# Kernel tuning notes

Hardware: AMD Instinct MI355X
Metric: run time of the kernel (lower is better)

Reference implementation:

```python
import jax, jax.numpy as jnp
import numpy as np

D_MODEL = 1024
N_HEADS = 16
D_K = D_MODEL // N_HEADS


def setup_inputs() -> dict:
    key = jax.random.key(0)
    ks = jax.random.split(key, 7)
    B, T = 4, 2048
    scale = 1.0 / np.sqrt(D_MODEL)
    x = jax.random.normal(ks[0], (B, T, D_MODEL), dtype=jnp.float32)
    Wq = jax.random.uniform(ks[1], (D_MODEL, D_MODEL), jnp.float32, -scale, scale)
    Wk = jax.random.uniform(ks[2], (D_MODEL, D_MODEL), jnp.float32, -scale, scale)
    Wv = jax.random.uniform(ks[3], (D_MODEL, D_MODEL), jnp.float32, -scale, scale)
    bq = jax.random.uniform(ks[4], (D_MODEL,), jnp.float32, -scale, scale)
    bk = jax.random.uniform(ks[5], (D_MODEL,), jnp.float32, -scale, scale)
    bv = jax.random.uniform(ks[6], (D_MODEL,), jnp.float32, -scale, scale)
    return {"x": x, "Wq": Wq, "bq": bq, "Wk": Wk, "bk": bk, "Wv": Wv, "bv": bv}


def reference(x, Wq, bq, Wk, bk, Wv, bv):
    B, T, _ = x.shape
    # QKV projections -> (B, H, T, d_k)
    def split_heads(y):
        return y.reshape(B, T, N_HEADS, D_K).transpose(0, 2, 1, 3)
    Q = split_heads(x @ Wq + bq)
    K = split_heads(x @ Wk + bk)
    V = split_heads(x @ Wv + bv)
    scores = jnp.einsum('bhqd,bhkd->bhqk', Q, K) / jnp.sqrt(jnp.float32(D_K))
    # additive causal mask: -inf above the diagonal
    causal = jnp.tril(jnp.ones((T, T), dtype=bool))
    scores = jnp.where(causal, scores, -jnp.inf)
    attn = jax.nn.softmax(scores, axis=-1)
    out = jnp.einsum('bhqk,bhkd->bhqd', attn, V)
    return out.transpose(0, 2, 1, 3).reshape(B, T, D_MODEL)
```

## Files before the change

kernel.cpp:

```cpp
#include <hip/hip_runtime.h>
#include <hip/hip_bf16.h>

#define DM 1024
#define NH 16
#define DK 64
#define TT 2048
#define NBATCH 4
#define BT 8192

typedef __attribute__((ext_vector_type(8))) short short8;
typedef __attribute__((ext_vector_type(4))) float f32x4;
typedef unsigned short u16;

#define MFMA(a,b,c) __builtin_amdgcn_mfma_f32_16x16x32_bf16((a),(b),(c),0,0,0)

#define QSCALE 0.18033688011112684f

#define EXP2(x) __builtin_amdgcn_exp2f(x)

__device__ __forceinline__ u16 f2bf(float f){
  union { float f; unsigned u; } v; v.f = f;
  return (u16)((v.u + 0x7fffu + ((v.u >> 16) & 1u)) >> 16);
}

__device__ __forceinline__ unsigned cvtpk(float lo, float hi){
  unsigned r;
  asm("v_cvt_pk_bf16_f32 %0, %1, %2" : "=v"(r) : "v"(lo), "v"(hi));
  return r;
}

__device__ __forceinline__ void gload16(const void* g, void* l){
  __builtin_amdgcn_global_load_lds((__attribute__((address_space(1))) void*)(g),
                                   (__attribute__((address_space(3))) void*)(l), 16, 0, 0);
}

__device__ __forceinline__ float plmax(float x){
#if __has_builtin(__builtin_amdgcn_permlane16_swap) && __has_builtin(__builtin_amdgcn_permlane32_swap)
  auto r = __builtin_amdgcn_permlane16_swap(__float_as_uint(x), __float_as_uint(x), false, false);
  x = fmaxf(__uint_as_float(r[0]), __uint_as_float(r[1]));
  auto r2 = __builtin_amdgcn_permlane32_swap(__float_as_uint(x), __float_as_uint(x), false, false);
  x = fmaxf(__uint_as_float(r2[0]), __uint_as_float(r2[1]));
#else
  x = fmaxf(x, __shfl_xor(x, 16, 64));
  x = fmaxf(x, __shfl_xor(x, 32, 64));
#endif
  return x;
}

__device__ __forceinline__ float plsum(float x){
#if __has_builtin(__builtin_amdgcn_permlane16_swap) && __has_builtin(__builtin_amdgcn_permlane32_swap)
  auto r = __builtin_amdgcn_permlane16_swap(__float_as_uint(x), __float_as_uint(x), false, false);
  x = __uint_as_float(r[0]) + __uint_as_float(r[1]);
  auto r2 = __builtin_amdgcn_permlane32_swap(__float_as_uint(x), __float_as_uint(x), false, false);
  x = __uint_as_float(r2[0]) + __uint_as_float(r2[1]);
#else
  x = x + __shfl_xor(x, 16, 64);
  x = x + __shfl_xor(x, 32, 64);
#endif
  return x;
}

__global__ __launch_bounds__(256) void cvt_x(const float* __restrict__ x, u16* __restrict__ xb){
  int i = (blockIdx.x * 256 + threadIdx.x) * 4;
  float4 v = *(const float4*)(x + i);
  u16 o0 = f2bf(v.x), o1 = f2bf(v.y), o2 = f2bf(v.z), o3 = f2bf(v.w);
  ushort4 o; o.x=o0; o.y=o1; o.z=o2; o.w=o3;
  *(ushort4*)(xb + i) = o;
}

__global__ __launch_bounds__(256) void twp(
    const float* __restrict__ Wq, const float* __restrict__ Wk, const float* __restrict__ Wv,
    u16* __restrict__ wtq, u16* __restrict__ wtk, u16* __restrict__ wtv){
  const float* W = (blockIdx.z == 0) ? Wq : (blockIdx.z == 1) ? Wk : Wv;
  u16* wt = (blockIdx.z == 0) ? wtq : (blockIdx.z == 1) ? wtk : wtv;
  __shared__ float tile[32][33];
  int k0 = blockIdx.x * 32, n0 = blockIdx.y * 32;
  int tx = threadIdx.x & 31, ty = threadIdx.x >> 5;
  #pragma unroll
  for(int r = ty; r < 32; r += 8)
    tile[r][tx] = W[(size_t)(k0 + r) * DM + n0 + tx];
  __syncthreads();
  #pragma unroll
  for(int r = ty; r < 32; r += 8)
    wt[(size_t)(n0 + r) * DM + k0 + tx] = f2bf(tile[tx][r]);
}

__global__ __launch_bounds__(256) void qkv_gemm(
    const u16* __restrict__ xb,
    const u16* __restrict__ wtq, const u16* __restrict__ wtk, const u16* __restrict__ wtv,
    const float* __restrict__ bq, const float* __restrict__ bk, const float* __restrict__ bv,
    u16* __restrict__ qws, u16* __restrict__ kws, u16* __restrict__ vtws){
  __shared__ u16 sa[128 * 64];
  __shared__ u16 sb[128 * 64];
  const int m0 = blockIdx.x * 128;
  const int ng = blockIdx.y * 128;
  const int mat = ng >> 10;
  const int n0 = ng & 1023;
  const u16* wt = (mat == 0) ? wtq : (mat == 1) ? wtk : wtv;
  const float* bias = (mat == 0) ? bq : (mat == 1) ? bk : bv;
  const int tid = threadIdx.x;
  const int lane = tid & 63, w = tid >> 6;
  const int wm = (w >> 1) * 64, wn = (w & 1) * 64;
  const int wbase0 = tid & 192;

  f32x4 acc[4][4] = {};

  for(int k0 = 0; k0 < 1024; k0 += 64){
    #pragma unroll
    for(int p = 0; p < 4; p++){
      int base = p * 256 + wbase0;
      int idx = base + lane;
      int row = idx >> 3;
      int chs = (idx & 7) ^ (row & 7);
      gload16(xb + (size_t)(m0 + row) * 1024 + k0 + chs * 8, (char*)sa + base * 16);
      gload16(wt + (size_t)(n0 + row) * 1024 + k0 + chs * 8, (char*)sb + base * 16);
    }
    __syncthreads();
    #pragma unroll
    for(int ks = 0; ks < 2; ks++){
      short8 af[4], bfr[4];
      #pragma unroll
      for(int i = 0; i < 4; i++){
        int ra = wm + i * 16 + (lane & 15);
        int ca = ks * 64 + (lane >> 4) * 16;
        af[i] = *(const short8*)((const char*)sa + ra * 128 + (ca ^ ((ra & 7) << 4)));
        int rb = wn + i * 16 + (lane & 15);
        bfr[i] = *(const short8*)((const char*)sb + rb * 128 + (ca ^ ((rb & 7) << 4)));
      }
      __builtin_amdgcn_s_setprio(1);
      #pragma unroll
      for(int i = 0; i < 4; i++)
        #pragma unroll
        for(int j = 0; j < 4; j++)
          acc[i][j] = MFMA(af[i], bfr[j], acc[i][j]);
      __builtin_amdgcn_s_setprio(0);
    }
    __syncthreads();
  }

  const float scl = (mat == 0) ? QSCALE : 1.0f;
  #pragma unroll
  for(int j = 0; j < 4; j++){
    int n = n0 + wn + j * 16 + (lane & 15);
    float bv_ = bias[n];
    int h = n >> 6, d = n & 63;
    #pragma unroll
    for(int i = 0; i < 4; i++){
      int mb = m0 + wm + i * 16 + (lane >> 4) * 4;
      int b = mb >> 11, t = mb & 2047;
      int bh = b * NH + h;
      if(mat == 2){
        ushort4 o4;
        o4.x = f2bf(acc[i][j][0] + bv_);
        o4.y = f2bf(acc[i][j][1] + bv_);
        o4.z = f2bf(acc[i][j][2] + bv_);
        o4.w = f2bf(acc[i][j][3] + bv_);
        int tp = (t & ~31) | (((t >> 2) & 3) << 3) | (((t >> 4) & 1) << 2);
        *(ushort4*)(vtws + ((size_t)bh * DK + d) * TT + tp) = o4;
      } else {
        u16* dst = (mat == 0) ? qws : kws;
        #pragma unroll
        for(int r = 0; r < 4; r++){
          u16 o = f2bf((acc[i][j][r] + bv_) * scl);
          dst[((size_t)bh * TT + t + r) * DK + d] = o;
        }
      }
    }
  }
}

__global__ __launch_bounds__(256) void attn(
    const u16* __restrict__ qws, const u16* __restrict__ kws, const u16* __restrict__ vtws,
    float* __restrict__ out){
  __shared__ u16 kt[2][64 * 64];
  __shared__ u16 vt[2][64 * 64];

  const int id = blockIdx.x;
  const int swz = (id & 7) * 128 + (id >> 3);
  const int qx = swz & 15;
  const int bh = swz >> 4;

  const int tid = threadIdx.x, lane = tid & 63, w = tid >> 6;
  const int g = lane >> 4, ln = lane & 15;
  const int b = bh >> 4, h = bh & 15;
  const u16* kbase = kws + (size_t)bh * TT * DK;
  const u16* vbase = vtws + (size_t)bh * DK * TT;
  const int wbase0 = tid & 192;

  #pragma unroll 1
  for(int qi = 0; qi < 2; qi++){
    const int qt = qi ? (31 - qx) : qx;
    const int q = qt * 64 + w * 16 + ln;

    short8 qf[2];
    {
      const u16* gq = qws + ((size_t)bh * TT + q) * DK + g * 8;
      qf[0] = *(const short8*)gq;
      qf[1] = *(const short8*)(gq + 32);
    }

    f32x4 o[4] = {};
    float m = -INFINITY, l = 0.f;

    const int nkt = qt + 1;

    __syncthreads();
    #pragma unroll
    for(int p = 0; p < 2; p++){
      int base = p * 256 + wbase0;
      int idx = base + lane, row = idx >> 3, chs = (idx & 7) ^ (row & 7);
      gload16(kbase + (size_t)row * DK + chs * 8, (char*)kt[0] + base * 16);
      gload16(vbase + (size_t)row * TT + chs * 8, (char*)vt[0] + base * 16);
    }

    #pragma unroll 1
    for(int kti = 0; kti < nkt; kti++){
      const int cur = kti & 1;
      __syncthreads();

      if(kti + 1 < nkt){
        const int k0n = (kti + 1) * 64;
        #pragma unroll
        for(int p = 0; p < 2; p++){
          int base = p * 256 + wbase0;
          int idx = base + lane, row = idx >> 3, chs = (idx & 7) ^ (row & 7);
          gload16(kbase + (size_t)(k0n + row) * DK + chs * 8, (char*)kt[cur ^ 1] + base * 16);
          gload16(vbase + (size_t)row * TT + k0n + chs * 8, (char*)vt[cur ^ 1] + base * 16);
        }
      }

      f32x4 s[4];
      __builtin_amdgcn_s_setprio(1);
      #pragma unroll
      for(int i = 0; i < 4; i++){
        f32x4 c = {};
        #pragma unroll
        for(int ks = 0; ks < 2; ks++){
          int rb = i * 16 + ln;
          int cb = ks * 64 + g * 16;
          short8 kfr = *(const short8*)((const char*)kt[cur] + rb * 128 + (cb ^ ((rb & 7) << 4)));
          c = MFMA(kfr, qf[ks], c);
        }
        s[i] = c;
      }
      __builtin_amdgcn_s_setprio(0);

      if(kti == nkt - 1){
        const int k0 = kti * 64;
        #pragma unroll
        for(int i = 0; i < 4; i++)
          #pragma unroll
          for(int r = 0; r < 4; r++)
            if(k0 + i * 16 + g * 4 + r > q) s[i][r] = -INFINITY;
      }

      float mx0 = fmaxf(fmaxf(s[0][0], s[0][1]), fmaxf(s[0][2], s[0][3]));
      float mx1 = fmaxf(fmaxf(s[1][0], s[1][1]), fmaxf(s[1][2], s[1][3]));
      float mx2 = fmaxf(fmaxf(s[2][0], s[2][1]), fmaxf(s[2][2], s[2][3]));
      float mx3 = fmaxf(fmaxf(s[3][0], s[3][1]), fmaxf(s[3][2], s[3][3]));
      float pmax = fmaxf(fmaxf(mx0, mx1), fmaxf(mx2, mx3));
      pmax = plmax(pmax);

      if(!__all(pmax <= m + 8.f)){
        float mnew = fmaxf(m, pmax);
        float alpha = EXP2(m - mnew);
        l *= alpha;
        #pragma unroll
        for(int i = 0; i < 4; i++)
          #pragma unroll
          for(int r = 0; r < 4; r++) o[i][r] *= alpha;
        m = mnew;
      }

      #pragma unroll
      for(int i = 0; i < 4; i++)
        #pragma unroll
        for(int r = 0; r < 4; r++){
          float p = EXP2(s[i][r] - m);
          s[i][r] = p; l += p;
        }

      union PU { short8 s8; unsigned w[4]; };
      PU pb[2];
      #pragma unroll
      for(int ks = 0; ks < 2; ks++){
        pb[ks].w[0] = cvtpk(s[2*ks][0],   s[2*ks][1]);
        pb[ks].w[1] = cvtpk(s[2*ks][2],   s[2*ks][3]);
        pb[ks].w[2] = cvtpk(s[2*ks+1][0], s[2*ks+1][1]);
        pb[ks].w[3] = cvtpk(s[2*ks+1][2], s[2*ks+1][3]);
      }

      __builtin_amdgcn_s_setprio(1);
      #pragma unroll
      for(int i = 0; i < 4; i++){
        int dr = i * 16 + ln;
        const char* vrow = (const char*)vt[cur] + dr * 128;
        int sw = (dr & 7) << 4;
        #pragma unroll
        for(int ks = 0; ks < 2; ks++){
          short8 av = *(const short8*)(vrow + ((64 * ks + g * 16) ^ sw));
          o[i] = MFMA(av, pb[ks].s8, o[i]);
        }
      }
      __builtin_amdgcn_s_setprio(0);
    }

    l = plsum(l);
    float inv = 1.0f / l;
    float* orow = out + ((size_t)(b * TT + q)) * DM + h * 64 + g * 4;
    #pragma unroll
    for(int i = 0; i < 4; i++){
      float4 v4;
      v4.x = o[i][0] * inv; v4.y = o[i][1] * inv;
      v4.z = o[i][2] * inv; v4.w = o[i][3] * inv;
      *(float4*)(orow + i * 16) = v4;
    }
  }
}

extern "C" void kernel_launch(void* const* d_in, const int* in_sizes, int n_in,
                              void* d_out, int out_size, void* d_ws, size_t ws_size,
                              hipStream_t stream){
  const float* x  = (const float*)d_in[0];
  const float* Wq = (const float*)d_in[1];
  const float* bq = (const float*)d_in[2];
  const float* Wk = (const float*)d_in[3];
  const float* bk = (const float*)d_in[4];
  const float* Wv = (const float*)d_in[5];
  const float* bv = (const float*)d_in[6];
  float* out = (float*)d_out;

  char* ws = (char*)d_ws;
  u16* xb   = (u16*)(ws);
  u16* wtq  = (u16*)(ws + (16u << 20));
  u16* wtk  = (u16*)(ws + (18u << 20));
  u16* wtv  = (u16*)(ws + (20u << 20));
  u16* qws  = (u16*)(ws + (22u << 20));
  u16* kws  = (u16*)(ws + (38u << 20));
  u16* vtws = (u16*)(ws + (54u << 20));

  cvt_x<<<dim3(BT * DM / 1024), dim3(256), 0, stream>>>(x, xb);
  twp<<<dim3(32, 32, 3), dim3(256), 0, stream>>>(Wq, Wk, Wv, wtq, wtk, wtv);
  qkv_gemm<<<dim3(64, 24), dim3(256), 0, stream>>>(xb, wtq, wtk, wtv, bq, bk, bv, qws, kws, vtws);
  attn<<<dim3(1024), dim3(256), 0, stream>>>(qws, kws, vtws, out);
}
```

Before: 156.4 us.

## Use 128-query attention tiles with 8 waves and swizzle GEMM block order

The attention kernel now runs 512 threads per block and covers 128 queries, so each K/V tile loaded into shared memory serves eight waves instead of four. This halves K/V global traffic per query and gives each thread a single 16-byte load per tile. The first four waves skip the final diagonal tile, which they do not need under the causal mask. The QKV GEMM launch is flattened to 1D with an XCD-aware swizzle of tile order, aimed at better L2 reuse. In exchange the grid is half as large and the last key tile leaves half the waves idle.

```diff
diff --git a/kernel.cpp b/kernel.cpp
--- a/kernel.cpp
+++ b/kernel.cpp
@@ -92,8 +92,12 @@
     u16* __restrict__ qws, u16* __restrict__ kws, u16* __restrict__ vtws){
   __shared__ u16 sa[128 * 64];
   __shared__ u16 sb[128 * 64];
-  const int m0 = blockIdx.x * 128;
-  const int ng = blockIdx.y * 128;
+  const int id = blockIdx.x;
+  const int idx = id >> 3;
+  const int mt = (id & 7) * 8 + (idx & 7);
+  const int y  = idx >> 3;
+  const int m0 = mt * 128;
+  const int ng = y * 128;
   const int mat = ng >> 10;
   const int n0 = ng & 1023;
   const u16* wt = (mat == 0) ? wtq : (mat == 1) ? wtk : wtv;
@@ -109,9 +113,9 @@
     #pragma unroll
     for(int p = 0; p < 4; p++){
       int base = p * 256 + wbase0;
-      int idx = base + lane;
-      int row = idx >> 3;
-      int chs = (idx & 7) ^ (row & 7);
+      int idx2 = base + lane;
+      int row = idx2 >> 3;
+      int chs = (idx2 & 7) ^ (row & 7);
       gload16(xb + (size_t)(m0 + row) * 1024 + k0 + chs * 8, (char*)sa + base * 16);
       gload16(wt + (size_t)(n0 + row) * 1024 + k0 + chs * 8, (char*)sb + base * 16);
     }
@@ -169,28 +173,30 @@
   }
 }
 
-__global__ __launch_bounds__(256) void attn(
+__global__ __launch_bounds__(512) void attn(
     const u16* __restrict__ qws, const u16* __restrict__ kws, const u16* __restrict__ vtws,
     float* __restrict__ out){
   __shared__ u16 kt[2][64 * 64];
   __shared__ u16 vt[2][64 * 64];
 
   const int id = blockIdx.x;
-  const int swz = (id & 7) * 128 + (id >> 3);
-  const int qx = swz & 15;
-  const int bh = swz >> 4;
+  const int swz = (id & 7) * 64 + (id >> 3);
+  const int qx = swz & 7;
+  const int bh = swz >> 3;
 
   const int tid = threadIdx.x, lane = tid & 63, w = tid >> 6;
   const int g = lane >> 4, ln = lane & 15;
   const int b = bh >> 4, h = bh & 15;
   const u16* kbase = kws + (size_t)bh * TT * DK;
   const u16* vbase = vtws + (size_t)bh * DK * TT;
-  const int wbase0 = tid & 192;
+  const int sbase = tid & 448;
+  const int srow = tid >> 3;
+  const int schs = (tid & 7) ^ (srow & 7);
 
   #pragma unroll 1
   for(int qi = 0; qi < 2; qi++){
-    const int qt = qi ? (31 - qx) : qx;
-    const int q = qt * 64 + w * 16 + ln;
+    const int qt = qi ? (15 - qx) : qx;
+    const int q = qt * 128 + w * 16 + ln;
 
     short8 qf[2];
     {
@@ -202,16 +208,12 @@
     f32x4 o[4] = {};
     float m = -INFINITY, l = 0.f;
 
-    const int nkt = qt + 1;
+    const int nkt = 2 * qt + 2;
+    const int myNkt = nkt - (w < 4 ? 1 : 0);
 
     __syncthreads();
-    #pragma unroll
-    for(int p = 0; p < 2; p++){
-      int base = p * 256 + wbase0;
-      int idx = base + lane, row = idx >> 3, chs = (idx & 7) ^ (row & 7);
-      gload16(kbase + (size_t)row * DK + chs * 8, (char*)kt[0] + base * 16);
-      gload16(vbase + (size_t)row * TT + chs * 8, (char*)vt[0] + base * 16);
-    }
+    gload16(kbase + (size_t)srow * DK + schs * 8, (char*)kt[0] + sbase * 16);
+    gload16(vbase + (size_t)srow * TT + schs * 8, (char*)vt[0] + sbase * 16);
 
     #pragma unroll 1
     for(int kti = 0; kti < nkt; kti++){
@@ -220,89 +222,86 @@
 
       if(kti + 1 < nkt){
         const int k0n = (kti + 1) * 64;
-        #pragma unroll
-        for(int p = 0; p < 2; p++){
-          int base = p * 256 + wbase0;
-          int idx = base + lane, row = idx >> 3, chs = (idx & 7) ^ (row & 7);
-          gload16(kbase + (size_t)(k0n + row) * DK + chs * 8, (char*)kt[cur ^ 1] + base * 16);
-          gload16(vbase + (size_t)row * TT + k0n + chs * 8, (char*)vt[cur ^ 1] + base * 16);
-        }
+        gload16(kbase + (size_t)(k0n + srow) * DK + schs * 8, (char*)kt[cur ^ 1] + sbase * 16);
+        gload16(vbase + (size_t)srow * TT + k0n + schs * 8, (char*)vt[cur ^ 1] + sbase * 16);
       }
 
-      f32x4 s[4];
-      __builtin_amdgcn_s_setprio(1);
-      #pragma unroll
-      for(int i = 0; i < 4; i++){
-        f32x4 c = {};
+      if(kti < myNkt){
+        f32x4 s[4];
+        __builtin_amdgcn_s_setprio(1);
+        #pragma unroll
+        for(int i = 0; i < 4; i++){
+          f32x4 c = {};
+          #pragma unroll
+          for(int ks = 0; ks < 2; ks++){
+            int rb = i * 16 + ln;
+            int cb = ks * 64 + g * 16;
+            short8 kfr = *(const short8*)((const char*)kt[cur] + rb * 128 + (cb ^ ((rb & 7) << 4)));
+            c = MFMA(kfr, qf[ks], c);
+          }
+          s[i] = c;
+        }
+        __builtin_amdgcn_s_setprio(0);
+
+        if(kti == myNkt - 1){
+          const int k0 = kti * 64;
+          #pragma unroll
+          for(int i = 0; i < 4; i++)
+            #pragma unroll
+            for(int r = 0; r < 4; r++)
+              if(k0 + i * 16 + g * 4 + r > q) s[i][r] = -INFINITY;
+        }
+
+        float mx0 = fmaxf(fmaxf(s[0][0], s[0][1]), fmaxf(s[0][2], s[0][3]));
+        float mx1 = fmaxf(fmaxf(s[1][0], s[1][1]), fmaxf(s[1][2], s[1][3]));
+        float mx2 = fmaxf(fmaxf(s[2][0], s[2][1]), fmaxf(s[2][2], s[2][3]));
+        float mx3 = fmaxf(fmaxf(s[3][0], s[3][1]), fmaxf(s[3][2], s[3][3]));
+        float pmax = fmaxf(fmaxf(mx0, mx1), fmaxf(mx2, mx3));
+        pmax = plmax(pmax);
+
+        if(!__all(pmax <= m + 8.f)){
+          float mnew = fmaxf(m, pmax);
+          float alpha = EXP2(m - mnew);
+          l *= alpha;
+          #pragma unroll
+          for(int i = 0; i < 4; i++)
+            #pragma unroll
+            for(int r = 0; r < 4; r++) o[i][r] *= alpha;
+          m = mnew;
+        }
+
+        #pragma unroll
+        for(int i = 0; i < 4; i++)
+          #pragma unroll
+          for(int r = 0; r < 4; r++){
+            float p = EXP2(s[i][r] - m);
+            s[i][r] = p; l += p;
+          }
+
+        union PU { short8 s8; unsigned w[4]; };
+        PU pb[2];
         #pragma unroll
         for(int ks = 0; ks < 2; ks++){
-          int rb = i * 16 + ln;
-          int cb = ks * 64 + g * 16;
-          short8 kfr = *(const short8*)((const char*)kt[cur] + rb * 128 + (cb ^ ((rb & 7) << 4)));
-          c = MFMA(kfr, qf[ks], c);
-        }
-        s[i] = c;
+          pb[ks].w[0] = cvtpk(s[2*ks][0],   s[2*ks][1]);
+          pb[ks].w[1] = cvtpk(s[2*ks][2],   s[2*ks][3]);
+          pb[ks].w[2] = cvtpk(s[2*ks+1][0], s[2*ks+1][1]);
+          pb[ks].w[3] = cvtpk(s[2*ks+1][2], s[2*ks+1][3]);
+        }
+
+        __builtin_amdgcn_s_setprio(1);
+        #pragma unroll
+        for(int i = 0; i < 4; i++){
+          int dr = i * 16 + ln;
+          const char* vrow = (const char*)vt[cur] + dr * 128;
+          int sw = (dr & 7) << 4;
+          #pragma unroll
+          for(int ks = 0; ks < 2; ks++){
+            short8 av = *(const short8*)(vrow + ((64 * ks + g * 16) ^ sw));
+            o[i] = MFMA(av, pb[ks].s8, o[i]);
+          }
+        }
+        __builtin_amdgcn_s_setprio(0);
       }
-      __builtin_amdgcn_s_setprio(0);
-
-      if(kti == nkt - 1){
-        const int k0 = kti * 64;
-        #pragma unroll
-        for(int i = 0; i < 4; i++)
-          #pragma unroll
-          for(int r = 0; r < 4; r++)
-            if(k0 + i * 16 + g * 4 + r > q) s[i][r] = -INFINITY;
-      }
-
-      float mx0 = fmaxf(fmaxf(s[0][0], s[0][1]), fmaxf(s[0][2], s[0][3]));
-      float mx1 = fmaxf(fmaxf(s[1][0], s[1][1]), fmaxf(s[1][2], s[1][3]));
-      float mx2 = fmaxf(fmaxf(s[2][0], s[2][1]), fmaxf(s[2][2], s[2][3]));
-      float mx3 = fmaxf(fmaxf(s[3][0], s[3][1]), fmaxf(s[3][2], s[3][3]));
-      float pmax = fmaxf(fmaxf(mx0, mx1), fmaxf(mx2, mx3));
-      pmax = plmax(pmax);
-
-      if(!__all(pmax <= m + 8.f)){
-        float mnew = fmaxf(m, pmax);
-        float alpha = EXP2(m - mnew);
-        l *= alpha;
-        #pragma unroll
-        for(int i = 0; i < 4; i++)
-          #pragma unroll
-          for(int r = 0; r < 4; r++) o[i][r] *= alpha;
-        m = mnew;
-      }
-
-      #pragma unroll
-      for(int i = 0; i < 4; i++)
-        #pragma unroll
-        for(int r = 0; r < 4; r++){
-          float p = EXP2(s[i][r] - m);
-          s[i][r] = p; l += p;
-        }
-
-      union PU { short8 s8; unsigned w[4]; };
-      PU pb[2];
-      #pragma unroll
-      for(int ks = 0; ks < 2; ks++){
-        pb[ks].w[0] = cvtpk(s[2*ks][0],   s[2*ks][1]);
-        pb[ks].w[1] = cvtpk(s[2*ks][2],   s[2*ks][3]);
-        pb[ks].w[2] = cvtpk(s[2*ks+1][0], s[2*ks+1][1]);
-        pb[ks].w[3] = cvtpk(s[2*ks+1][2], s[2*ks+1][3]);
-      }
-
-      __builtin_amdgcn_s_setprio(1);
-      #pragma unroll
-      for(int i = 0; i < 4; i++){
-        int dr = i * 16 + ln;
-        const char* vrow = (const char*)vt[cur] + dr * 128;
-        int sw = (dr & 7) << 4;
-        #pragma unroll
-        for(int ks = 0; ks < 2; ks++){
-          short8 av = *(const short8*)(vrow + ((64 * ks + g * 16) ^ sw));
-          o[i] = MFMA(av, pb[ks].s8, o[i]);
-        }
-      }
-      __builtin_amdgcn_s_setprio(0);
     }
 
     l = plsum(l);
@@ -341,6 +340,6 @@
 
   cvt_x<<<dim3(BT * DM / 1024), dim3(256), 0, stream>>>(x, xb);
   twp<<<dim3(32, 32, 3), dim3(256), 0, stream>>>(Wq, Wk, Wv, wtq, wtk, wtv);
-  qkv_gemm<<<dim3(64, 24), dim3(256), 0, stream>>>(xb, wtq, wtk, wtv, bq, bk, bv, qws, kws, vtws);
-  attn<<<dim3(1024), dim3(256), 0, stream>>>(qws, kws, vtws, out);
-}
+  qkv_gemm<<<dim3(1536), dim3(256), 0, stream>>>(xb, wtq, wtk, wtv, bq, bk, bv, qws, kws, vtws);
+  attn<<<dim3(512), dim3(512), 0, stream>>>(qws, kws, vtws, out);
+}
```

Measured after the change: 147.7 us. -5.6%, faster.
